# Optimization experiments

Hardware: AMD Instinct MI355X
Metric: run time of the kernel (lower is better)

The kernel has to match this reference:

```python
import jax, jax.numpy as jnp
import numpy as np

B, T, D = 4, 4096, 512
H, L = 8, 6
HD = D // H
BS = 64          # block_size
MLP = 2048
VOCAB = 96000
MAX_SCALE = 10000.0
LN_EPS = 1e-6


def _sinusoidal_pe(length, dim, max_scale=MAX_SCALE):
    # flax common_layers sinusoidal init (concat sin|cos halves)
    pos = np.arange(length)[:, None].astype(np.float32)
    div = np.exp(np.arange(0, dim, 2).astype(np.float32) * -(np.log(max_scale) / dim))
    pe = np.zeros((length, dim), dtype=np.float32)
    pe[:, : dim // 2] = np.sin(pos * div)
    pe[:, dim // 2:] = np.cos(pos * div)
    return jnp.asarray(pe)

_PE = _sinusoidal_pe(T, D)


def layer_norm(x, scale, bias):
    m = jnp.mean(x, axis=-1, keepdims=True)
    v = jnp.mean(jnp.square(x - m), axis=-1, keepdims=True)
    return (x - m) * jax.lax.rsqrt(v + LN_EPS) * scale + bias


def local_block_attention(x, mask, wq, wk, wv, wo, stagger):
    # x: [B, T, D], mask: [B, T] bool (True = real token)
    b, t, d = x.shape
    if stagger:
        lp = BS // 2
        rp = BS - lp
        x = jnp.pad(x, ((0, 0), (lp, rp), (0, 0)))
        mask = jnp.pad(mask, ((0, 0), (lp, rp)))
    tp = x.shape[1]
    nb = tp // BS
    xb = x.reshape(b, nb, BS, d)          # [B, nb, BS, D]
    mb = mask.reshape(b, nb, BS)          # [B, nb, BS]
    scale = 1.0 / float(np.sqrt(HD))
    q = jnp.einsum('bnsd,dhf->bnshf', xb, wq) * scale
    k = jnp.einsum('bnsd,dhf->bnshf', xb, wk)
    v = jnp.einsum('bnsd,dhf->bnshf', xb, wv)
    scores = jnp.einsum('bnqhf,bnkhf->bnhqk', q, k)       # [B, nb, H, BS, BS]
    scores = jnp.where(mb[:, :, None, None, :], scores, jnp.asarray(-1e9, scores.dtype))
    probs = jax.nn.softmax(scores, axis=-1)
    o = jnp.einsum('bnhqk,bnkhf->bnqhf', probs, v)
    o = jnp.einsum('bnqhf,hfd->bnqd', o, wo).reshape(b, tp, d)
    if stagger:
        o = o[:, lp:lp + t]
    return o


def setup_inputs() -> dict:
    key = jax.random.key(0)
    ks = jax.random.split(key, 10)
    inputs = jax.random.randint(ks[0], (B, T), 0, VOCAB)
    embed = jax.random.normal(ks[1], (VOCAB, D), dtype=jnp.float32)
    s = 0.02
    wq = jax.random.normal(ks[2], (L, D, H, HD), dtype=jnp.float32) * s
    wk = jax.random.normal(ks[3], (L, D, H, HD), dtype=jnp.float32) * s
    wv = jax.random.normal(ks[4], (L, D, H, HD), dtype=jnp.float32) * s
    wo = jax.random.normal(ks[5], (L, H, HD, D), dtype=jnp.float32) * s
    w1 = jax.random.normal(ks[6], (L, D, MLP), dtype=jnp.float32) * s
    b1 = jnp.zeros((L, MLP), dtype=jnp.float32)
    w2 = jax.random.normal(ks[7], (L, MLP, D), dtype=jnp.float32) * s
    b2 = jnp.zeros((L, D), dtype=jnp.float32)
    ln1_s = jnp.ones((L, D), dtype=jnp.float32)
    ln1_b = jnp.zeros((L, D), dtype=jnp.float32)
    ln2_s = jnp.ones((L, D), dtype=jnp.float32)
    ln2_b = jnp.zeros((L, D), dtype=jnp.float32)
    lnf_s = jnp.ones((D,), dtype=jnp.float32)
    lnf_b = jnp.zeros((D,), dtype=jnp.float32)
    return {'inputs': inputs, 'embed': embed, 'wq': wq, 'wk': wk, 'wv': wv, 'wo': wo,
            'ln1_s': ln1_s, 'ln1_b': ln1_b, 'ln2_s': ln2_s, 'ln2_b': ln2_b,
            'w1': w1, 'b1': b1, 'w2': w2, 'b2': b2, 'lnf_s': lnf_s, 'lnf_b': lnf_b}


def reference(inputs, embed, wq, wk, wv, wo, ln1_s, ln1_b, ln2_s, ln2_b,
              w1, b1, w2, b2, lnf_s, lnf_b):
    mask = inputs > 0                      # src padding mask [B, T]
    x = embed[inputs.astype(jnp.int32)]    # [B, T, D]
    x = x + _PE[None, :, :]                # sinusoidal position embedding
    for lyr in range(L):
        stagger = (lyr % 2 == 1)           # stagger_local_blocks on odd layers
        h = layer_norm(x, ln1_s[lyr], ln1_b[lyr])
        h = local_block_attention(h, mask, wq[lyr], wk[lyr], wv[lyr], wo[lyr], stagger)
        x = x + h
        y = layer_norm(x, ln2_s[lyr], ln2_b[lyr])
        y = jnp.matmul(jax.nn.relu(jnp.matmul(y, w1[lyr]) + b1[lyr]), w2[lyr]) + b2[lyr]
        x = x + y
    return layer_norm(x, lnf_s, lnf_b)
```

## Files before the change

kernel.cpp:

```cpp
#include <hip/hip_runtime.h>

typedef unsigned short u16;
typedef unsigned int   u32;
typedef __attribute__((ext_vector_type(8))) short short8;
typedef __attribute__((ext_vector_type(4))) float f32x4;

#define TSEQ   4096
#define DMODEL 512
#define NHEAD  8
#define HDIM   64
#define NLAYER 6
#define MLPD   2048

#define GPTR(p) (const __attribute__((address_space(1))) void*)(p)
#define LPTR(p) (__attribute__((address_space(3))) void*)(p)

__device__ __forceinline__ u16 f2b(float f) {
  u32 u = __float_as_uint(f);
  u32 r = (u + 0x7fffu + ((u >> 16) & 1u)) >> 16;
  return (u16)r;
}
__device__ __forceinline__ float b2f(u16 h) { return __uint_as_float(((u32)h) << 16); }

__device__ __forceinline__ short8 ld8g(const u16* p, bool ok) {
  if (ok) return *(const short8*)p;
  short8 z = {0, 0, 0, 0, 0, 0, 0, 0};
  return z;
}

__global__ __launch_bounds__(256) void transpose_convert_all(
    const float* __restrict__ wq, const float* __restrict__ wk,
    const float* __restrict__ wv, const float* __restrict__ wo,
    const float* __restrict__ w1, const float* __restrict__ w2,
    u16* __restrict__ wqkv_bt, u16* __restrict__ wo_bt,
    u16* __restrict__ w1_bt, u16* __restrict__ w2_bt) {
  __shared__ float tile[64][65];
  int bx = blockIdx.x, l = blockIdx.y;
  const float* W; u16* out; int K, N, Ntot, ro, kb, nb2;
  if (bx < 256) {
    int which = bx >> 6, local = bx & 63;
    K = 512; N = 512; kb = local & 7; nb2 = local >> 3;
    if (which == 0)      { W = wq; out = wqkv_bt; Ntot = 1536; ro = 0; }
    else if (which == 1) { W = wk; out = wqkv_bt; Ntot = 1536; ro = 512; }
    else if (which == 2) { W = wv; out = wqkv_bt; Ntot = 1536; ro = 1024; }
    else                 { W = wo; out = wo_bt;   Ntot = 512;  ro = 0; }
  } else if (bx < 512) {
    int local = bx - 256;
    W = w1; out = w1_bt; K = 512; N = 2048; Ntot = 2048; ro = 0;
    kb = local & 7; nb2 = local >> 3;
  } else {
    int local = bx - 512;
    W = w2; out = w2_bt; K = 2048; N = 512; Ntot = 512; ro = 0;
    kb = local >> 3; nb2 = local & 7;
  }
  int k0 = kb * 64, n0 = nb2 * 64;
  const float* Wl = W + (size_t)l * K * N;
  u16* Ol = out + (size_t)l * Ntot * K;
  int tx = threadIdx.x & 15, ty = threadIdx.x >> 4;
#pragma unroll
  for (int p = 0; p < 4; ++p) {
    int k = k0 + p * 16 + ty;
    float4 v = *(const float4*)(Wl + (size_t)k * N + n0 + tx * 4);
    tile[p * 16 + ty][tx * 4 + 0] = v.x;
    tile[p * 16 + ty][tx * 4 + 1] = v.y;
    tile[p * 16 + ty][tx * 4 + 2] = v.z;
    tile[p * 16 + ty][tx * 4 + 3] = v.w;
  }
  __syncthreads();
#pragma unroll
  for (int p = 0; p < 4; ++p) {
    int n = n0 + p * 16 + ty;
    ushort4 s;
    s.x = f2b(tile[tx * 4 + 0][p * 16 + ty]);
    s.y = f2b(tile[tx * 4 + 1][p * 16 + ty]);
    s.z = f2b(tile[tx * 4 + 2][p * 16 + ty]);
    s.w = f2b(tile[tx * 4 + 3][p * 16 + ty]);
    *(ushort4*)(Ol + (size_t)(ro + n) * K + k0 + tx * 4) = s;
  }
}

__global__ void embed_pe_kernel(const int* __restrict__ idx,
                                const float* __restrict__ embed,
                                float* __restrict__ x) {
  int i = blockIdx.x;
  int t = i & (TSEQ - 1);
  int tok = idx[i];
  int c = threadIdx.x * 4;
  float4 e = *(const float4*)(embed + (size_t)tok * DMODEL + c);
  float vals[4] = {e.x, e.y, e.z, e.w};
  float o[4];
#pragma unroll
  for (int j = 0; j < 4; ++j) {
    int col = c + j;
    int jj = (col < 256) ? col : col - 256;
    float div = __expf((float)jj * -0.035977892078032f);
    float arg = (float)t * div;
    o[j] = vals[j] + ((col < 256) ? __sinf(arg) : __cosf(arg));
  }
  float4 r = {o[0], o[1], o[2], o[3]};
  *(float4*)(x + (size_t)i * DMODEL + c) = r;
}

template <bool OUT_BF16>
__global__ __launch_bounds__(256) void ln_kernel(
    const float* __restrict__ x, const float* __restrict__ gamma,
    const float* __restrict__ beta, void* __restrict__ out) {
  int wave = threadIdx.x >> 6, lane = threadIdx.x & 63;
  int row = (blockIdx.x << 2) + wave;
  const float* xr = x + (size_t)row * DMODEL + lane * 8;
  float4 a = *(const float4*)xr;
  float4 b = *(const float4*)(xr + 4);
  float v[8] = {a.x, a.y, a.z, a.w, b.x, b.y, b.z, b.w};
  float s = 0.f;
#pragma unroll
  for (int j = 0; j < 8; ++j) s += v[j];
#pragma unroll
  for (int off = 1; off < 64; off <<= 1) s += __shfl_xor(s, off, 64);
  float mean = s * (1.0f / 512.0f);
  float q = 0.f;
#pragma unroll
  for (int j = 0; j < 8; ++j) { float d = v[j] - mean; q += d * d; }
#pragma unroll
  for (int off = 1; off < 64; off <<= 1) q += __shfl_xor(q, off, 64);
  float rstd = rsqrtf(q * (1.0f / 512.0f) + 1e-6f);
  float4 g0 = *(const float4*)(gamma + lane * 8);
  float4 g1 = *(const float4*)(gamma + lane * 8 + 4);
  float4 p0 = *(const float4*)(beta + lane * 8);
  float4 p1 = *(const float4*)(beta + lane * 8 + 4);
  float g[8] = {g0.x, g0.y, g0.z, g0.w, g1.x, g1.y, g1.z, g1.w};
  float be[8] = {p0.x, p0.y, p0.z, p0.w, p1.x, p1.y, p1.z, p1.w};
  float r[8];
#pragma unroll
  for (int j = 0; j < 8; ++j) r[j] = (v[j] - mean) * rstd * g[j] + be[j];
  if (OUT_BF16) {
    uint4 pk;
    pk.x = (u32)f2b(r[0]) | ((u32)f2b(r[1]) << 16);
    pk.y = (u32)f2b(r[2]) | ((u32)f2b(r[3]) << 16);
    pk.z = (u32)f2b(r[4]) | ((u32)f2b(r[5]) << 16);
    pk.w = (u32)f2b(r[6]) | ((u32)f2b(r[7]) << 16);
    *(uint4*)((u16*)out + (size_t)row * DMODEL + lane * 8) = pk;
  } else {
    float4 r0 = {r[0], r[1], r[2], r[3]};
    float4 r1 = {r[4], r[5], r[6], r[7]};
    float* op = (float*)out + (size_t)row * DMODEL + lane * 8;
    *(float4*)op = r0;
    *(float4*)(op + 4) = r1;
  }
}

template <int FLAGS>
__global__ __launch_bounds__(256) void gemm_kernel(
    const u16* __restrict__ A, const u16* __restrict__ Bt,
    const float* __restrict__ bias, const float* __restrict__ resid,
    void* __restrict__ out, void* __restrict__ out2, int M, int N, int K) {
  __shared__ __align__(16) u16 a_lds[3][128][32];
  __shared__ __align__(16) u16 b_lds[3][128][32];
  int m0 = blockIdx.y * 128, n0 = blockIdx.x * 128;
  int t = threadIdx.x;
  int lr = t >> 2, lc = (t & 3) * 8;
  int wave = t >> 6, lane = t & 63;
  int wm = (wave >> 1) * 64, wn = (wave & 1) * 64;
  int fr = lane & 15, quad = lane >> 4;

  f32x4 acc[4][4];
  f32x4 zz = {0.f, 0.f, 0.f, 0.f};
#pragma unroll
  for (int i = 0; i < 4; ++i)
#pragma unroll
    for (int j = 0; j < 4; ++j) acc[i][j] = zz;

  const u16* Ag0 = A + (size_t)(m0 + lr) * K + lc;
  const u16* Ag1 = A + (size_t)(m0 + lr + 64) * K + lc;
  const u16* Bg0 = Bt + (size_t)(n0 + lr) * K + lc;
  const u16* Bg1 = Bt + (size_t)(n0 + lr + 64) * K + lc;

  __builtin_amdgcn_global_load_lds(GPTR(Ag0), LPTR(&a_lds[0][lr][lc]), 16, 0, 0);
  __builtin_amdgcn_global_load_lds(GPTR(Ag1), LPTR(&a_lds[0][lr + 64][lc]), 16, 0, 0);
  __builtin_amdgcn_global_load_lds(GPTR(Bg0), LPTR(&b_lds[0][lr][lc]), 16, 0, 0);
  __builtin_amdgcn_global_load_lds(GPTR(Bg1), LPTR(&b_lds[0][lr + 64][lc]), 16, 0, 0);

  int T = K >> 5;
  int buf = 0;
  for (int tt = 0; tt < T; ++tt) {
    int nb = buf + 1 == 3 ? 0 : buf + 1;
    if (tt + 1 < T) {
      int off = (tt + 1) << 5;
      __builtin_amdgcn_global_load_lds(GPTR(Ag0 + off), LPTR(&a_lds[nb][lr][lc]), 16, 0, 0);
      __builtin_amdgcn_global_load_lds(GPTR(Ag1 + off), LPTR(&a_lds[nb][lr + 64][lc]), 16, 0, 0);
      __builtin_amdgcn_global_load_lds(GPTR(Bg0 + off), LPTR(&b_lds[nb][lr][lc]), 16, 0, 0);
      __builtin_amdgcn_global_load_lds(GPTR(Bg1 + off), LPTR(&b_lds[nb][lr + 64][lc]), 16, 0, 0);
      asm volatile("s_waitcnt vmcnt(4)\n\ts_barrier" ::: "memory");
    } else {
      asm volatile("s_waitcnt vmcnt(0)\n\ts_barrier" ::: "memory");
    }
    short8 af[4], bf[4];
#pragma unroll
    for (int mi = 0; mi < 4; ++mi)
      af[mi] = *(const short8*)&a_lds[buf][wm + mi * 16 + fr][quad * 8];
#pragma unroll
    for (int ni = 0; ni < 4; ++ni)
      bf[ni] = *(const short8*)&b_lds[buf][wn + ni * 16 + fr][quad * 8];
#pragma unroll
    for (int mi = 0; mi < 4; ++mi)
#pragma unroll
      for (int ni = 0; ni < 4; ++ni)
        acc[mi][ni] = __builtin_amdgcn_mfma_f32_16x16x32_bf16(
            af[mi], bf[ni], acc[mi][ni], 0, 0, 0);
    buf = nb;
  }

  if (FLAGS & 16) {
#pragma unroll
    for (int mi = 0; mi < 4; ++mi)
#pragma unroll
      for (int ni = 0; ni < 4; ++ni) {
        int colg = n0 + wn + ni * 16 + fr;
        if (colg < 1024) {
#pragma unroll
          for (int r = 0; r < 4; ++r) {
            int rowg = m0 + wm + mi * 16 + quad * 4 + r;
            ((u16*)out)[(size_t)rowg * 1024 + colg] = f2b(acc[mi][ni][r]);
          }
        } else {
          int hh = (colg - 1024) >> 6, ff = colg & 63;
          int rowg0 = m0 + wm + mi * 16 + quad * 4;
          int bb = rowg0 >> 12, tok = rowg0 & 4095;
          ushort4 pk;
          pk.x = f2b(acc[mi][ni][0]);
          pk.y = f2b(acc[mi][ni][1]);
          pk.z = f2b(acc[mi][ni][2]);
          pk.w = f2b(acc[mi][ni][3]);
          *(ushort4*)((u16*)out2 +
                      ((size_t)(bb * 8 + hh) * 64 + ff) * 4096 + tok) = pk;
        }
      }
    return;
  }

#pragma unroll
  for (int mi = 0; mi < 4; ++mi)
#pragma unroll
    for (int ni = 0; ni < 4; ++ni) {
      int colg = n0 + wn + ni * 16 + fr;
      float bv = (FLAGS & 1) ? bias[colg] : 0.0f;
#pragma unroll
      for (int r = 0; r < 4; ++r) {
        int rowg = m0 + wm + mi * 16 + quad * 4 + r;
        float val = acc[mi][ni][r] + bv;
        if (FLAGS & 2) val = fmaxf(val, 0.0f);
        if (FLAGS & 4) val += resid[(size_t)rowg * N + colg];
        if (FLAGS & 8)
          ((u16*)out)[(size_t)rowg * N + colg] = f2b(val);
        else
          ((float*)out)[(size_t)rowg * N + colg] = val;
      }
    }
}

__global__ __launch_bounds__(128) void attn_mfma_kernel(
    const u16* __restrict__ qk, const u16* __restrict__ vt,
    const int* __restrict__ tokens, u16* __restrict__ o, int sh) {
  __shared__ __align__(16) u16 ps[2][64][72];
  __shared__ float kmask[64];
  int n = blockIdx.x, hg = blockIdx.y, b = blockIdx.z;
  int tid = threadIdx.x;
  int w = tid >> 6, lane = tid & 63;
  int head = hg * 2 + w;
  int fr = lane & 15, quad = lane >> 4;

  if (tid < 64) {
    int pp = n * 64 + tid - sh;
    kmask[tid] =
        (pp >= 0 && pp < TSEQ && tokens[(size_t)b * TSEQ + pp] > 0) ? 1.f : 0.f;
  }
  __syncthreads();

  const u16* qkb = qk + (size_t)b * TSEQ * 1024;

  f32x4 st[4][4];
  f32x4 zz = {0.f, 0.f, 0.f, 0.f};
#pragma unroll
  for (int i = 0; i < 4; ++i)
#pragma unroll
    for (int j = 0; j < 4; ++j) st[i][j] = zz;
#pragma unroll
  for (int kk = 0; kk < 2; ++kk) {
    short8 ka[4], qb[4];
#pragma unroll
    for (int mi = 0; mi < 4; ++mi) {
      int p = n * 64 + mi * 16 + fr - sh;
      ka[mi] = ld8g(qkb + (ptrdiff_t)p * 1024 + 512 + head * 64 + kk * 32 + quad * 8,
                    p >= 0 && p < TSEQ);
    }
#pragma unroll
    for (int ni = 0; ni < 4; ++ni) {
      int p = n * 64 + ni * 16 + fr - sh;
      qb[ni] = ld8g(qkb + (ptrdiff_t)p * 1024 + head * 64 + kk * 32 + quad * 8,
                    p >= 0 && p < TSEQ);
    }
#pragma unroll
    for (int mi = 0; mi < 4; ++mi)
#pragma unroll
      for (int ni = 0; ni < 4; ++ni)
        st[mi][ni] = __builtin_amdgcn_mfma_f32_16x16x32_bf16(
            ka[mi], qb[ni], st[mi][ni], 0, 0, 0);
  }

  float kmv[4][4];
#pragma unroll
  for (int mi = 0; mi < 4; ++mi)
#pragma unroll
    for (int r = 0; r < 4; ++r) kmv[mi][r] = kmask[mi * 16 + quad * 4 + r];
#pragma unroll
  for (int ni = 0; ni < 4; ++ni) {
    float mx = -3.0e38f;
#pragma unroll
    for (int mi = 0; mi < 4; ++mi)
#pragma unroll
      for (int r = 0; r < 4; ++r) {
        float s = (kmv[mi][r] > 0.f) ? st[mi][ni][r] * 0.125f : -1.0e9f;
        st[mi][ni][r] = s;
        mx = fmaxf(mx, s);
      }
    mx = fmaxf(mx, __shfl_xor(mx, 16, 64));
    mx = fmaxf(mx, __shfl_xor(mx, 32, 64));
    float sm = 0.f;
#pragma unroll
    for (int mi = 0; mi < 4; ++mi)
#pragma unroll
      for (int r = 0; r < 4; ++r) {
        float e = __expf(st[mi][ni][r] - mx);
        st[mi][ni][r] = e;
        sm += e;
      }
    sm += __shfl_xor(sm, 16, 64);
    sm += __shfl_xor(sm, 32, 64);
    float inv = 1.0f / sm;
#pragma unroll
    for (int mi = 0; mi < 4; ++mi)
#pragma unroll
      for (int r = 0; r < 4; ++r) st[mi][ni][r] *= inv;
  }

#pragma unroll
  for (int mi = 0; mi < 4; ++mi)
#pragma unroll
    for (int ni = 0; ni < 4; ++ni) {
      uint2 pk;
      pk.x = (u32)f2b(st[mi][ni][0]) | ((u32)f2b(st[mi][ni][1]) << 16);
      pk.y = (u32)f2b(st[mi][ni][2]) | ((u32)f2b(st[mi][ni][3]) << 16);
      *(uint2*)&ps[w][ni * 16 + fr][mi * 16 + quad * 4] = pk;
    }
  __syncthreads();

  f32x4 oc[4][4];
#pragma unroll
  for (int i = 0; i < 4; ++i)
#pragma unroll
    for (int j = 0; j < 4; ++j) oc[i][j] = zz;
  const u16* vtb = vt + (size_t)(b * 8 + head) * 64 * 4096;
#pragma unroll
  for (int kk = 0; kk < 2; ++kk) {
    short8 pa[4], vb[4];
#pragma unroll
    for (int mi = 0; mi < 4; ++mi)
      pa[mi] = *(const short8*)&ps[w][mi * 16 + fr][kk * 32 + quad * 8];
    int key0 = n * 64 - sh + kk * 32 + quad * 8;
    bool kok = (key0 >= 0) && (key0 < TSEQ);
#pragma unroll
    for (int ni = 0; ni < 4; ++ni)
      vb[ni] = ld8g(vtb + (size_t)(ni * 16 + fr) * 4096 + key0, kok);
#pragma unroll
    for (int mi = 0; mi < 4; ++mi)
#pragma unroll
      for (int ni = 0; ni < 4; ++ni)
        oc[mi][ni] = __builtin_amdgcn_mfma_f32_16x16x32_bf16(
            pa[mi], vb[ni], oc[mi][ni], 0, 0, 0);
  }

#pragma unroll
  for (int mi = 0; mi < 4; ++mi)
#pragma unroll
    for (int ni = 0; ni < 4; ++ni)
#pragma unroll
      for (int r = 0; r < 4; ++r) {
        int q = mi * 16 + quad * 4 + r;
        int p = n * 64 + q - sh;
        if (p >= 0 && p < TSEQ)
          o[((size_t)(b * TSEQ + p)) * DMODEL + head * 64 + ni * 16 + fr] =
              f2b(oc[mi][ni][r]);
      }
}

extern "C" void kernel_launch(void* const* d_in, const int* in_sizes, int n_in,
                              void* d_out, int out_size, void* d_ws, size_t ws_size,
                              hipStream_t stream) {
  (void)in_sizes; (void)n_in; (void)out_size; (void)ws_size;
  const int*   tokens = (const int*)d_in[0];
  const float* embed  = (const float*)d_in[1];
  const float* wq = (const float*)d_in[2];
  const float* wk = (const float*)d_in[3];
  const float* wv = (const float*)d_in[4];
  const float* wo = (const float*)d_in[5];
  const float* ln1_s = (const float*)d_in[6];
  const float* ln1_b = (const float*)d_in[7];
  const float* ln2_s = (const float*)d_in[8];
  const float* ln2_b = (const float*)d_in[9];
  const float* w1 = (const float*)d_in[10];
  const float* b1 = (const float*)d_in[11];
  const float* w2 = (const float*)d_in[12];
  const float* b2 = (const float*)d_in[13];
  const float* lnf_s = (const float*)d_in[14];
  const float* lnf_b = (const float*)d_in[15];

  char* ws = (char*)d_ws;
  const size_t MB = 1024ull * 1024ull;
  float* x     = (float*)(ws + 0);
  u16* h       = (u16*)(ws + 32 * MB);
  u16* qk      = (u16*)(ws + 48 * MB);
  u16* vt      = (u16*)(ws + 82 * MB);
  u16* obuf    = (u16*)(ws + 99 * MB);
  u16* hidden  = (u16*)(ws + 48 * MB);
  u16* wqkv_bt = (u16*)(ws + 116 * MB);
  u16* wo_bt   = (u16*)(ws + 126 * MB);
  u16* w1_bt   = (u16*)(ws + 130 * MB);
  u16* w2_bt   = (u16*)(ws + 143 * MB);

  transpose_convert_all<<<dim3(768, 6), 256, 0, stream>>>(
      wq, wk, wv, wo, w1, w2, wqkv_bt, wo_bt, w1_bt, w2_bt);

  embed_pe_kernel<<<16384, 128, 0, stream>>>(tokens, embed, x);

  for (int l = 0; l < NLAYER; ++l) {
    int sh = (l & 1) ? 32 : 0;
    int nb = (l & 1) ? 65 : 64;
    ln_kernel<true><<<4096, 256, 0, stream>>>(x, ln1_s + l * 512, ln1_b + l * 512, h);
    gemm_kernel<16><<<dim3(12, 128), 256, 0, stream>>>(
        h, wqkv_bt + (size_t)l * 1536 * 512, nullptr, nullptr, qk, vt,
        16384, 1536, 512);
    attn_mfma_kernel<<<dim3(nb, 4, 4), 128, 0, stream>>>(qk, vt, tokens, obuf, sh);
    gemm_kernel<4><<<dim3(4, 128), 256, 0, stream>>>(
        obuf, wo_bt + (size_t)l * 512 * 512, nullptr, x, x, nullptr,
        16384, 512, 512);
    ln_kernel<true><<<4096, 256, 0, stream>>>(x, ln2_s + l * 512, ln2_b + l * 512, h);
    gemm_kernel<1 | 2 | 8><<<dim3(16, 128), 256, 0, stream>>>(
        h, w1_bt + (size_t)l * 2048 * 512, b1 + l * 2048, nullptr, hidden, nullptr,
        16384, 2048, 512);
    gemm_kernel<1 | 4><<<dim3(4, 128), 256, 0, stream>>>(
        hidden, w2_bt + (size_t)l * 512 * 2048, b2 + l * 512, x, x, nullptr,
        16384, 512, 2048);
  }
  ln_kernel<false><<<4096, 256, 0, stream>>>(x, lnf_s, lnf_b, d_out);
}
```

Baseline: 1.568 ms.

## Add 256x256-tile GEMM kernel with 8 waves for QKV and MLP-up projections

Introduces a new GEMM kernel that computes a 256x256 output tile per workgroup with 512 threads. It double-buffers LDS through direct global-to-LDS loads and interleaves staging of the next tile with MFMA work, using barriers and s_setprio. The QKV and first MLP projections now use it, aiming for more data reuse per tile and better overlap of loads with math. The cost is a much larger LDS footprint and register use per block, and fewer blocks in the grid, which could hurt occupancy or load balance.

```diff
diff --git a/kernel.cpp b/kernel.cpp
--- a/kernel.cpp
+++ b/kernel.cpp
@@ -257,6 +257,171 @@
     }
 }
 
+template <int FLAGS>
+__global__ __launch_bounds__(512, 2) void gemm256_kernel(
+    const u16* __restrict__ A, const u16* __restrict__ Bt,
+    const float* __restrict__ bias, const float* __restrict__ resid,
+    void* __restrict__ out, void* __restrict__ out2, int M, int N, int K) {
+  __shared__ __align__(16) u16 a_lds[2][16384];
+  __shared__ __align__(16) u16 b_lds[2][16384];
+  int m0 = blockIdx.y * 256, n0 = blockIdx.x * 256;
+  int tid = threadIdx.x;
+  int w = tid >> 6, lane = tid & 63;
+  int fr = lane & 15, quad = lane >> 4;
+  int wms = (w >> 2) * 8;
+  int wns = (w & 3) * 4;
+  int rS = lane >> 2;
+  int cS = ((lane & 3) * 8) ^ ((lane & 32) ? 16 : 0);
+  const u16* Asrc = A + (size_t)(m0 + w * 16 + rS) * K + cS;
+  const u16* Bsrc = Bt + (size_t)(n0 + w * 16 + rS) * K + cS;
+  int wBase = w * 1024 + lane * 8;
+  int rdoff = fr * 32 + ((quad * 8) ^ ((fr & 8) ? 16 : 0));
+  int NT = K >> 6;
+
+  f32x4 acc[8][4];
+  f32x4 zz = {0.f, 0.f, 0.f, 0.f};
+#pragma unroll
+  for (int i = 0; i < 8; ++i)
+#pragma unroll
+    for (int j = 0; j < 4; ++j) acc[i][j] = zz;
+
+  auto stage_half = [&](int hh) {
+    if (hh >= 4 * NT) return;
+    int th = hh >> 2, part = hh & 3, kk = part >> 1;
+    const u16* src = (part & 1) ? Bsrc : Asrc;
+    u16* ldsb = (part & 1) ? &b_lds[0][0] : &a_lds[0][0];
+    ldsb += (size_t)(th & 1) * 16384;
+    src += (size_t)th * 64 + kk * 32;
+#pragma unroll
+    for (int j = 0; j < 2; ++j) {
+      __builtin_amdgcn_global_load_lds(GPTR(src + (size_t)j * 128 * K),
+                                       LPTR(ldsb + kk * 512 + j * 8192 + wBase),
+                                       16, 0, 0);
+    }
+  };
+
+#pragma unroll
+  for (int hh = 0; hh < 6; ++hh) stage_half(hh);
+  asm volatile("s_waitcnt vmcnt(4)\n\ts_barrier" ::: "memory");
+
+  for (int t = 0; t < NT; ++t) {
+    const u16* ap = a_lds[t & 1];
+    const u16* bp = b_lds[t & 1];
+    short8 aF[4], bF[4];
+#define LDA256(mi_, kk_) (*(const short8*)&ap[((wms + (mi_)) * 2 + (kk_)) * 512 + rdoff])
+#define LDB256(ni_, kk_) (*(const short8*)&bp[((wns + (ni_)) * 2 + (kk_)) * 512 + rdoff])
+#pragma unroll
+    for (int ni = 0; ni < 4; ++ni) bF[ni] = LDB256(ni, 0);
+#pragma unroll
+    for (int mi = 0; mi < 4; ++mi) aF[mi] = LDA256(mi, 0);
+    stage_half(4 * t + 6);
+    __builtin_amdgcn_s_barrier();
+    __builtin_amdgcn_s_setprio(1);
+#pragma unroll
+    for (int mi = 0; mi < 4; ++mi)
+#pragma unroll
+      for (int ni = 0; ni < 4; ++ni)
+        acc[mi][ni] = __builtin_amdgcn_mfma_f32_16x16x32_bf16(
+            aF[mi], bF[ni], acc[mi][ni], 0, 0, 0);
+    __builtin_amdgcn_s_setprio(0);
+    __builtin_amdgcn_s_barrier();
+#pragma unroll
+    for (int mi = 0; mi < 4; ++mi) aF[mi] = LDA256(4 + mi, 0);
+    stage_half(4 * t + 7);
+    __builtin_amdgcn_s_barrier();
+    __builtin_amdgcn_s_setprio(1);
+#pragma unroll
+    for (int mi = 0; mi < 4; ++mi)
+#pragma unroll
+      for (int ni = 0; ni < 4; ++ni)
+        acc[4 + mi][ni] = __builtin_amdgcn_mfma_f32_16x16x32_bf16(
+            aF[mi], bF[ni], acc[4 + mi][ni], 0, 0, 0);
+    __builtin_amdgcn_s_setprio(0);
+    __builtin_amdgcn_s_barrier();
+#pragma unroll
+    for (int ni = 0; ni < 4; ++ni) bF[ni] = LDB256(ni, 1);
+#pragma unroll
+    for (int mi = 0; mi < 4; ++mi) aF[mi] = LDA256(mi, 1);
+    stage_half(4 * t + 8);
+    __builtin_amdgcn_s_barrier();
+    __builtin_amdgcn_s_setprio(1);
+#pragma unroll
+    for (int mi = 0; mi < 4; ++mi)
+#pragma unroll
+      for (int ni = 0; ni < 4; ++ni)
+        acc[mi][ni] = __builtin_amdgcn_mfma_f32_16x16x32_bf16(
+            aF[mi], bF[ni], acc[mi][ni], 0, 0, 0);
+    __builtin_amdgcn_s_setprio(0);
+    __builtin_amdgcn_s_barrier();
+#pragma unroll
+    for (int mi = 0; mi < 4; ++mi) aF[mi] = LDA256(4 + mi, 1);
+    stage_half(4 * t + 9);
+    __builtin_amdgcn_s_barrier();
+    __builtin_amdgcn_s_setprio(1);
+#pragma unroll
+    for (int mi = 0; mi < 4; ++mi)
+#pragma unroll
+      for (int ni = 0; ni < 4; ++ni)
+        acc[4 + mi][ni] = __builtin_amdgcn_mfma_f32_16x16x32_bf16(
+            aF[mi], bF[ni], acc[4 + mi][ni], 0, 0, 0);
+    __builtin_amdgcn_s_setprio(0);
+    if (t + 2 == NT)
+      asm volatile("s_waitcnt vmcnt(0)\n\ts_barrier" ::: "memory");
+    else if (t + 1 < NT)
+      asm volatile("s_waitcnt vmcnt(4)\n\ts_barrier" ::: "memory");
+#undef LDA256
+#undef LDB256
+  }
+
+  int wm = (w >> 2) * 128, wn = (w & 3) * 64;
+  if (FLAGS & 16) {
+#pragma unroll
+    for (int mi = 0; mi < 8; ++mi)
+#pragma unroll
+      for (int ni = 0; ni < 4; ++ni) {
+        int colg = n0 + wn + ni * 16 + fr;
+        if (colg < 1024) {
+#pragma unroll
+          for (int r = 0; r < 4; ++r) {
+            int rowg = m0 + wm + mi * 16 + quad * 4 + r;
+            ((u16*)out)[(size_t)rowg * 1024 + colg] = f2b(acc[mi][ni][r]);
+          }
+        } else {
+          int hh = (colg - 1024) >> 6, ff = colg & 63;
+          int rowg0 = m0 + wm + mi * 16 + quad * 4;
+          int bb2 = rowg0 >> 12, tok = rowg0 & 4095;
+          ushort4 pk;
+          pk.x = f2b(acc[mi][ni][0]);
+          pk.y = f2b(acc[mi][ni][1]);
+          pk.z = f2b(acc[mi][ni][2]);
+          pk.w = f2b(acc[mi][ni][3]);
+          *(ushort4*)((u16*)out2 +
+                      ((size_t)(bb2 * 8 + hh) * 64 + ff) * 4096 + tok) = pk;
+        }
+      }
+    return;
+  }
+
+#pragma unroll
+  for (int mi = 0; mi < 8; ++mi)
+#pragma unroll
+    for (int ni = 0; ni < 4; ++ni) {
+      int colg = n0 + wn + ni * 16 + fr;
+      float bv = (FLAGS & 1) ? bias[colg] : 0.0f;
+#pragma unroll
+      for (int r = 0; r < 4; ++r) {
+        int rowg = m0 + wm + mi * 16 + quad * 4 + r;
+        float val = acc[mi][ni][r] + bv;
+        if (FLAGS & 2) val = fmaxf(val, 0.0f);
+        if (FLAGS & 4) val += resid[(size_t)rowg * N + colg];
+        if (FLAGS & 8)
+          ((u16*)out)[(size_t)rowg * N + colg] = f2b(val);
+        else
+          ((float*)out)[(size_t)rowg * N + colg] = val;
+      }
+    }
+}
+
 __global__ __launch_bounds__(128) void attn_mfma_kernel(
     const u16* __restrict__ qk, const u16* __restrict__ vt,
     const int* __restrict__ tokens, u16* __restrict__ o, int sh) {
@@ -435,7 +600,7 @@
     int sh = (l & 1) ? 32 : 0;
     int nb = (l & 1) ? 65 : 64;
     ln_kernel<true><<<4096, 256, 0, stream>>>(x, ln1_s + l * 512, ln1_b + l * 512, h);
-    gemm_kernel<16><<<dim3(12, 128), 256, 0, stream>>>(
+    gemm256_kernel<16><<<dim3(6, 64), 512, 0, stream>>>(
         h, wqkv_bt + (size_t)l * 1536 * 512, nullptr, nullptr, qk, vt,
         16384, 1536, 512);
     attn_mfma_kernel<<<dim3(nb, 4, 4), 128, 0, stream>>>(qk, vt, tokens, obuf, sh);
@@ -443,7 +608,7 @@
         obuf, wo_bt + (size_t)l * 512 * 512, nullptr, x, x, nullptr,
         16384, 512, 512);
     ln_kernel<true><<<4096, 256, 0, stream>>>(x, ln2_s + l * 512, ln2_b + l * 512, h);
-    gemm_kernel<1 | 2 | 8><<<dim3(16, 128), 256, 0, stream>>>(
+    gemm256_kernel<1 | 2 | 8><<<dim3(8, 64), 512, 0, stream>>>(
         h, w1_bt + (size_t)l * 2048 * 512, b1 + l * 2048, nullptr, hidden, nullptr,
         16384, 2048, 512);
     gemm_kernel<1 | 4><<<dim3(4, 128), 256, 0, stream>>>(
```

Result: slower. 1.600 ms, median of 2 (+2.0%).
